# Optimization experiments

Measured on AMD Instinct MI355X. Metric: run time of the kernel, lower is better.

Reference implementation:

```python
import jax, jax.numpy as jnp
import numpy as np

N = 100000      # kg_E, number of entities
D = 256         # rel_dim
E = 1600000     # total COO edges (all batches concatenated)


def setup_inputs() -> dict:
    key = jax.random.key(0)
    ks = jax.random.split(key, 8)
    right_embed = jax.random.normal(ks[0], (N, D), dtype=jnp.float32)
    W1 = jax.random.normal(ks[1], (D, D), dtype=jnp.float32) * 0.02
    Wr = jax.random.normal(ks[2], (D, D), dtype=jnp.float32) * 0.02
    br = jax.random.normal(ks[3], (D,), dtype=jnp.float32) * 0.02
    edge_vals = jax.random.uniform(ks[4], (E,), dtype=jnp.float32)  # 1/(deg+1) weights
    edge_rows = jnp.sort(jax.random.randint(ks[5], (E,), 0, N))
    edge_cols = jax.random.randint(ks[6], (E,), 0, N)
    perm = jax.random.randint(ks[7], (N,), 0, N)  # ent_newid_tensor
    return {"right_embed": right_embed, "W1": W1, "Wr": Wr, "br": br,
            "edge_vals": edge_vals, "edge_rows": edge_rows,
            "edge_cols": edge_cols, "perm": perm}


def reference(right_embed, W1, Wr, br, edge_vals, edge_rows, edge_cols, perm):
    # add_diag_layer: dense transform then normalized-adjacency SpMM + ReLU
    h = right_embed @ W1                                   # [N, D]
    msg = edge_vals[:, None] * h[edge_cols]                # [E, D] gather
    agg = jax.ops.segment_sum(msg, edge_rows, num_segments=N)  # scatter-add
    gcn_e_1 = jax.nn.relu(agg)                             # [N, D]
    # highway gate blend with permuted input embeddings
    left = right_embed[perm]                               # [N, D]
    gate = jax.nn.sigmoid(left @ Wr + br)                  # [N, D]
    return gate * gcn_e_1 + (1.0 - gate) * left
```

## Files before the change

kernel.cpp:

```cpp
#include <hip/hip_runtime.h>
#include <hip/hip_bf16.h>
#include <math.h>

#define D 256

typedef short s16x8 __attribute__((ext_vector_type(8)));
typedef float f32x4 __attribute__((ext_vector_type(4)));

__device__ __forceinline__ unsigned short f2bf(float f) {
    unsigned int u = __builtin_bit_cast(unsigned int, f);
    unsigned int r = (u + 0x7fffu + ((u >> 16) & 1u)) >> 16;
    return (unsigned short)r;
}
__device__ __forceinline__ float bf2f(unsigned short s) {
    unsigned int u = ((unsigned int)s) << 16;
    return __builtin_bit_cast(float, u);
}

__global__ void pre_all(const float* __restrict__ X,
                        const float* __restrict__ W1, const float* __restrict__ Wr,
                        unsigned short* __restrict__ Xbf,
                        unsigned short* __restrict__ W1sw, unsigned short* __restrict__ Wrsw,
                        const int* __restrict__ rows, int* __restrict__ rp,
                        int N, int E, int rpBlocks) {
    int bid = blockIdx.x;
    if (bid < 512) {
        int idx = bid * 256 + threadIdx.x;
        int m = idx >> 16;
        int t = idx & 65535;
        const float* src = m ? Wr : W1;
        unsigned short* dst = m ? Wrsw : W1sw;
        int j = t & 7, lane = (t >> 3) & 63, nt = (t >> 9) & 15, kt = t >> 13;
        int k = kt * 32 + (lane >> 4) * 8 + j;
        int n = nt * 16 + (lane & 15);
        dst[t] = f2bf(src[k * D + n]);
    } else if (bid < 512 + rpBlocks) {
        int r = (bid - 512) * 256 + threadIdx.x;
        if (r > N) return;
        int lo = 0, hi = E;
        while (lo < hi) {
            int mid = (lo + hi) >> 1;
            if (rows[mid] < r) lo = mid + 1; else hi = mid;
        }
        rp[r] = lo;
    } else {
        long long c = (long long)(bid - 512 - rpBlocks) * 256 + threadIdx.x;
        long long i8 = c * 8;
        if (i8 >= (long long)N * D) return;
        float4 f0 = *(const float4*)(X + i8);
        float4 f1 = *(const float4*)(X + i8 + 4);
        s16x8 sf;
        sf[0] = (short)f2bf(f0.x); sf[1] = (short)f2bf(f0.y);
        sf[2] = (short)f2bf(f0.z); sf[3] = (short)f2bf(f0.w);
        sf[4] = (short)f2bf(f1.x); sf[5] = (short)f2bf(f1.y);
        sf[6] = (short)f2bf(f1.z); sf[7] = (short)f2bf(f1.w);
        *(s16x8*)(Xbf + i8) = sf;
    }
}

__device__ __forceinline__ void acc4(float4& a, uint2 u, float v) {
    float x0 = __builtin_bit_cast(float, u.x << 16);
    float x1 = __builtin_bit_cast(float, u.x & 0xffff0000u);
    float x2 = __builtin_bit_cast(float, u.y << 16);
    float x3 = __builtin_bit_cast(float, u.y & 0xffff0000u);
    a.x += v * x0; a.y += v * x1; a.z += v * x2; a.w += v * x3;
}

__global__ __launch_bounds__(256) void scatter_x(const uint2* __restrict__ xp,
                                                 const int* __restrict__ rp,
                                                 const int* __restrict__ cols,
                                                 const float* __restrict__ vals,
                                                 uint2* __restrict__ aggp,
                                                 int N, int E) {
    int lane = threadIdx.x & 63;
    int wave = threadIdx.x >> 6;
    int row = blockIdx.x * 4 + wave;
    if (row >= N) return;
    int start = rp[row], end = rp[row + 1];

    float4 a = {0.f, 0.f, 0.f, 0.f};
    for (int base = start; base < end; base += 64) {
        int ii = base + lane;
        int iic = ii < E ? ii : E - 1;
        int cl = cols[iic];
        int vbits = __builtin_bit_cast(int, vals[iic]);
        int n = end - base; if (n > 64) n = 64;
        int i = 0;
        for (; i + 8 <= n; i += 8) {
            uint2 u[8]; float vv[8];
#pragma unroll
            for (int k = 0; k < 8; k++) {
                int c = __builtin_amdgcn_readlane(cl, i + k);
                vv[k] = __builtin_bit_cast(float, __builtin_amdgcn_readlane(vbits, i + k));
                u[k] = xp[(size_t)c * 64 + lane];
            }
#pragma unroll
            for (int k = 0; k < 8; k++) acc4(a, u[k], vv[k]);
        }
        for (; i < n; i++) {
            int c = __builtin_amdgcn_readlane(cl, i);
            float v = __builtin_bit_cast(float, __builtin_amdgcn_readlane(vbits, i));
            uint2 u = xp[(size_t)c * 64 + lane];
            acc4(a, u, v);
        }
    }
    uint2 o;
    o.x = (unsigned int)f2bf(a.x) | ((unsigned int)f2bf(a.y) << 16);
    o.y = (unsigned int)f2bf(a.z) | ((unsigned int)f2bf(a.w) << 16);
    aggp[(size_t)row * 64 + lane] = o;
}

__global__ __launch_bounds__(512, 4) void gemm_ff(const unsigned short* __restrict__ aggX,
                                                  const unsigned short* __restrict__ Xbf,
                                                  const int* __restrict__ perm,
                                                  const unsigned short* __restrict__ W1sw,
                                                  const unsigned short* __restrict__ Wrsw,
                                                  const float* __restrict__ br,
                                                  float* __restrict__ out,
                                                  int N, int numTiles) {
    __shared__ unsigned short lA[8 * 64 * 16];
    int t = threadIdx.x;
    int lane = t & 63;
    int wave = t >> 6;
    int quad = lane >> 4;
    int tile = blockIdx.x;
    if (tile >= numTiles) return;

#pragma unroll
    for (int q = 0; q < 2; q++) {
        int fgi = q * 512 + t;
        int mt = fgi >> 9, kt = (fgi >> 6) & 7, ll = fgi & 63;
        int rl = ll & 15, qd = ll >> 4;
        int grow = tile * 32 + mt * 16 + rl;
        if (grow >= N) grow = N - 1;
        int pr = perm[grow];
        *(s16x8*)(lA + (size_t)fgi * 8) = *(const s16x8*)(Xbf + (size_t)pr * D + kt * 32 + qd * 8);
    }

    s16x8 bfr[2][8];
#pragma unroll
    for (int ntl = 0; ntl < 2; ntl++) {
        int nt = wave * 2 + ntl;
#pragma unroll
        for (int kt = 0; kt < 8; kt++)
            bfr[ntl][kt] = *(const s16x8*)(W1sw + ((size_t)((kt * 16 + nt) * 64 + lane)) * 8);
    }
    f32x4 acc1[2][2];
#pragma unroll
    for (int mt = 0; mt < 2; mt++)
#pragma unroll
        for (int ntl = 0; ntl < 2; ntl++) acc1[mt][ntl] = (f32x4){0.f, 0.f, 0.f, 0.f};

#pragma unroll
    for (int mt = 0; mt < 2; mt++) {
        int grow = tile * 32 + mt * 16 + (lane & 15);
        if (grow >= N) grow = N - 1;
        const unsigned short* ap = aggX + (size_t)grow * D + (lane >> 4) * 8;
#pragma unroll
        for (int kt = 0; kt < 8; kt++) {
            s16x8 a = *(const s16x8*)(ap + kt * 32);
            acc1[mt][0] = __builtin_amdgcn_mfma_f32_16x16x32_bf16(a, bfr[0][kt], acc1[mt][0], 0, 0, 0);
            acc1[mt][1] = __builtin_amdgcn_mfma_f32_16x16x32_bf16(a, bfr[1][kt], acc1[mt][1], 0, 0, 0);
        }
    }
    __syncthreads();

#pragma unroll
    for (int ntl = 0; ntl < 2; ntl++) {
        int nt = wave * 2 + ntl;
#pragma unroll
        for (int kt = 0; kt < 8; kt++)
            bfr[ntl][kt] = *(const s16x8*)(Wrsw + ((size_t)((kt * 16 + nt) * 64 + lane)) * 8);
    }
    f32x4 acc2[2][2];
#pragma unroll
    for (int mt = 0; mt < 2; mt++)
#pragma unroll
        for (int ntl = 0; ntl < 2; ntl++) acc2[mt][ntl] = (f32x4){0.f, 0.f, 0.f, 0.f};

#pragma unroll
    for (int mt = 0; mt < 2; mt++)
#pragma unroll
        for (int kt = 0; kt < 8; kt++) {
            s16x8 a = *(const s16x8*)(lA + (size_t)(((mt * 8 + kt) * 64 + lane)) * 8);
            acc2[mt][0] = __builtin_amdgcn_mfma_f32_16x16x32_bf16(a, bfr[0][kt], acc2[mt][0], 0, 0, 0);
            acc2[mt][1] = __builtin_amdgcn_mfma_f32_16x16x32_bf16(a, bfr[1][kt], acc2[mt][1], 0, 0, 0);
        }

#pragma unroll
    for (int mt = 0; mt < 2; mt++) {
#pragma unroll
        for (int ntl = 0; ntl < 2; ntl++) {
            int col = (wave * 2 + ntl) * 16 + (lane & 15);
            float b = br[col];
            int kt2 = col >> 5, qd2 = (col >> 3) & 3, j2 = col & 7;
#pragma unroll
            for (int r = 0; r < 4; r++) {
                int rt = mt * 16 + quad * 4 + r;
                int grow = tile * 32 + rt;
                if (grow < N) {
                    float pre = acc2[mt][ntl][r] + b;
                    float gate = 1.f / (1.f + __expf(-pre));
                    float gcn = fmaxf(acc1[mt][ntl][r], 0.f);
                    float left = bf2f(lA[(size_t)(((mt * 8 + kt2) * 64 + qd2 * 16 + (rt & 15))) * 8 + j2]);
                    out[(size_t)grow * D + col] = gate * gcn + (1.f - gate) * left;
                }
            }
        }
    }
}

extern "C" void kernel_launch(void* const* d_in, const int* in_sizes, int n_in,
                              void* d_out, int out_size, void* d_ws, size_t ws_size,
                              hipStream_t stream) {
    const float* right = (const float*)d_in[0];
    const float* W1    = (const float*)d_in[1];
    const float* Wr    = (const float*)d_in[2];
    const float* br    = (const float*)d_in[3];
    const float* evals = (const float*)d_in[4];
    const int*   erows = (const int*)d_in[5];
    const int*   ecols = (const int*)d_in[6];
    const int*   perm  = (const int*)d_in[7];
    int N = in_sizes[7];
    int E = in_sizes[4];
    float* out = (float*)d_out;

    char* ws = (char*)d_ws;
    unsigned short* W1sw = (unsigned short*)ws;
    unsigned short* Wrsw = W1sw + D * D;
    int* rp = (int*)(ws + (size_t)2 * D * D * 2);
    size_t off = (size_t)2 * D * D * 2 + 4 * (size_t)(N + 1);
    off = (off + 255) & ~(size_t)255;
    unsigned short* Xbf = (unsigned short*)(ws + off);
    unsigned short* aggX = Xbf + (size_t)N * D;

    int numTiles = (N + 31) / 32;
    int rpBlocks = (N + 256) / 256;
    long long cvtElems = (long long)N * D / 8;
    int cvtBlocks = (int)((cvtElems + 255) / 256);

    pre_all<<<512 + rpBlocks + cvtBlocks, 256, 0, stream>>>(right, W1, Wr, Xbf, W1sw, Wrsw,
                                                            erows, rp, N, E, rpBlocks);
    scatter_x<<<(N + 3) / 4, 256, 0, stream>>>((const uint2*)Xbf, rp, ecols, evals,
                                               (uint2*)aggX, N, E);
    gemm_ff<<<numTiles, 512, 0, stream>>>(aggX, Xbf, perm, W1sw, Wrsw, br, out, N, numTiles);
}
```

Before: 395.1 us.

## Process two row tiles per block in fused GEMM to reuse weight fragments

Each block of the final fused kernel now handles two 32-row tiles instead of one. W1 and Wr fragments are loaded into registers once and used for both tiles, halving weight-load traffic per tile. The ReLU'd first-GEMM result is packed to bf16 in registers so both tiles' outputs can be kept until the gate phase. This adds LDS use (two tiles of gathered rows), rounds the GCN term to bf16, and drops the occupancy hint, which may cut the number of resident blocks.

```diff
diff --git a/kernel.cpp b/kernel.cpp
--- a/kernel.cpp
+++ b/kernel.cpp
@@ -110,31 +110,35 @@
     aggp[(size_t)row * 64 + lane] = o;
 }
 
-__global__ __launch_bounds__(512, 4) void gemm_ff(const unsigned short* __restrict__ aggX,
-                                                  const unsigned short* __restrict__ Xbf,
-                                                  const int* __restrict__ perm,
-                                                  const unsigned short* __restrict__ W1sw,
-                                                  const unsigned short* __restrict__ Wrsw,
-                                                  const float* __restrict__ br,
-                                                  float* __restrict__ out,
-                                                  int N, int numTiles) {
-    __shared__ unsigned short lA[8 * 64 * 16];
+__global__ __launch_bounds__(512) void gemm_ff2(const unsigned short* __restrict__ aggX,
+                                                const unsigned short* __restrict__ Xbf,
+                                                const int* __restrict__ perm,
+                                                const unsigned short* __restrict__ W1sw,
+                                                const unsigned short* __restrict__ Wrsw,
+                                                const float* __restrict__ br,
+                                                float* __restrict__ out,
+                                                int N, int numTiles) {
+    __shared__ unsigned short lA[2][8192];
     int t = threadIdx.x;
     int lane = t & 63;
     int wave = t >> 6;
     int quad = lane >> 4;
-    int tile = blockIdx.x;
-    if (tile >= numTiles) return;
-
-#pragma unroll
-    for (int q = 0; q < 2; q++) {
-        int fgi = q * 512 + t;
-        int mt = fgi >> 9, kt = (fgi >> 6) & 7, ll = fgi & 63;
-        int rl = ll & 15, qd = ll >> 4;
-        int grow = tile * 32 + mt * 16 + rl;
-        if (grow >= N) grow = N - 1;
-        int pr = perm[grow];
-        *(s16x8*)(lA + (size_t)fgi * 8) = *(const s16x8*)(Xbf + (size_t)pr * D + kt * 32 + qd * 8);
+    int t0 = blockIdx.x * 2;
+    int nT = (t0 + 1 < numTiles) ? 2 : 1;
+
+    for (int tt = 0; tt < nT; tt++) {
+        int tile = t0 + tt;
+#pragma unroll
+        for (int q = 0; q < 2; q++) {
+            int fgi = q * 512 + t;
+            int mt = fgi >> 9, kt = (fgi >> 6) & 7, ll = fgi & 63;
+            int rl = ll & 15, qd = ll >> 4;
+            int grow = tile * 32 + mt * 16 + rl;
+            if (grow >= N) grow = N - 1;
+            int pr = perm[grow];
+            *(s16x8*)(&lA[tt][(size_t)fgi * 8]) =
+                *(const s16x8*)(Xbf + (size_t)pr * D + kt * 32 + qd * 8);
+        }
     }
 
     s16x8 bfr[2][8];
@@ -145,25 +149,39 @@
         for (int kt = 0; kt < 8; kt++)
             bfr[ntl][kt] = *(const s16x8*)(W1sw + ((size_t)((kt * 16 + nt) * 64 + lane)) * 8);
     }
-    f32x4 acc1[2][2];
-#pragma unroll
-    for (int mt = 0; mt < 2; mt++)
-#pragma unroll
-        for (int ntl = 0; ntl < 2; ntl++) acc1[mt][ntl] = (f32x4){0.f, 0.f, 0.f, 0.f};
-
-#pragma unroll
-    for (int mt = 0; mt < 2; mt++) {
-        int grow = tile * 32 + mt * 16 + (lane & 15);
-        if (grow >= N) grow = N - 1;
-        const unsigned short* ap = aggX + (size_t)grow * D + (lane >> 4) * 8;
-#pragma unroll
-        for (int kt = 0; kt < 8; kt++) {
-            s16x8 a = *(const s16x8*)(ap + kt * 32);
-            acc1[mt][0] = __builtin_amdgcn_mfma_f32_16x16x32_bf16(a, bfr[0][kt], acc1[mt][0], 0, 0, 0);
-            acc1[mt][1] = __builtin_amdgcn_mfma_f32_16x16x32_bf16(a, bfr[1][kt], acc1[mt][1], 0, 0, 0);
-        }
-    }
-    __syncthreads();
+
+    unsigned int g1[2][8];
+    for (int tt = 0; tt < nT; tt++) {
+        int tile = t0 + tt;
+        f32x4 acc[2][2];
+#pragma unroll
+        for (int mt = 0; mt < 2; mt++)
+#pragma unroll
+            for (int ntl = 0; ntl < 2; ntl++) acc[mt][ntl] = (f32x4){0.f, 0.f, 0.f, 0.f};
+#pragma unroll
+        for (int mt = 0; mt < 2; mt++) {
+            int grow = tile * 32 + mt * 16 + (lane & 15);
+            if (grow >= N) grow = N - 1;
+            const unsigned short* ap = aggX + (size_t)grow * D + (lane >> 4) * 8;
+#pragma unroll
+            for (int kt = 0; kt < 8; kt++) {
+                s16x8 a = *(const s16x8*)(ap + kt * 32);
+                acc[mt][0] = __builtin_amdgcn_mfma_f32_16x16x32_bf16(a, bfr[0][kt], acc[mt][0], 0, 0, 0);
+                acc[mt][1] = __builtin_amdgcn_mfma_f32_16x16x32_bf16(a, bfr[1][kt], acc[mt][1], 0, 0, 0);
+            }
+        }
+#pragma unroll
+        for (int mt = 0; mt < 2; mt++)
+#pragma unroll
+            for (int ntl = 0; ntl < 2; ntl++)
+#pragma unroll
+                for (int rp2 = 0; rp2 < 2; rp2++) {
+                    float e0 = fmaxf(acc[mt][ntl][2 * rp2], 0.f);
+                    float e1 = fmaxf(acc[mt][ntl][2 * rp2 + 1], 0.f);
+                    g1[tt][(mt * 2 + ntl) * 2 + rp2] =
+                        (unsigned int)f2bf(e0) | ((unsigned int)f2bf(e1) << 16);
+                }
+    }
 
 #pragma unroll
     for (int ntl = 0; ntl < 2; ntl++) {
@@ -172,38 +190,42 @@
         for (int kt = 0; kt < 8; kt++)
             bfr[ntl][kt] = *(const s16x8*)(Wrsw + ((size_t)((kt * 16 + nt) * 64 + lane)) * 8);
     }
-    f32x4 acc2[2][2];
-#pragma unroll
-    for (int mt = 0; mt < 2; mt++)
-#pragma unroll
-        for (int ntl = 0; ntl < 2; ntl++) acc2[mt][ntl] = (f32x4){0.f, 0.f, 0.f, 0.f};
-
-#pragma unroll
-    for (int mt = 0; mt < 2; mt++)
-#pragma unroll
-        for (int kt = 0; kt < 8; kt++) {
-            s16x8 a = *(const s16x8*)(lA + (size_t)(((mt * 8 + kt) * 64 + lane)) * 8);
-            acc2[mt][0] = __builtin_amdgcn_mfma_f32_16x16x32_bf16(a, bfr[0][kt], acc2[mt][0], 0, 0, 0);
-            acc2[mt][1] = __builtin_amdgcn_mfma_f32_16x16x32_bf16(a, bfr[1][kt], acc2[mt][1], 0, 0, 0);
-        }
-
-#pragma unroll
-    for (int mt = 0; mt < 2; mt++) {
-#pragma unroll
-        for (int ntl = 0; ntl < 2; ntl++) {
-            int col = (wave * 2 + ntl) * 16 + (lane & 15);
-            float b = br[col];
-            int kt2 = col >> 5, qd2 = (col >> 3) & 3, j2 = col & 7;
-#pragma unroll
-            for (int r = 0; r < 4; r++) {
-                int rt = mt * 16 + quad * 4 + r;
-                int grow = tile * 32 + rt;
-                if (grow < N) {
-                    float pre = acc2[mt][ntl][r] + b;
-                    float gate = 1.f / (1.f + __expf(-pre));
-                    float gcn = fmaxf(acc1[mt][ntl][r], 0.f);
-                    float left = bf2f(lA[(size_t)(((mt * 8 + kt2) * 64 + qd2 * 16 + (rt & 15))) * 8 + j2]);
-                    out[(size_t)grow * D + col] = gate * gcn + (1.f - gate) * left;
+    __syncthreads();
+
+    for (int tt = 0; tt < nT; tt++) {
+        int tile = t0 + tt;
+        f32x4 acc[2][2];
+#pragma unroll
+        for (int mt = 0; mt < 2; mt++)
+#pragma unroll
+            for (int ntl = 0; ntl < 2; ntl++) acc[mt][ntl] = (f32x4){0.f, 0.f, 0.f, 0.f};
+#pragma unroll
+        for (int mt = 0; mt < 2; mt++)
+#pragma unroll
+            for (int kt = 0; kt < 8; kt++) {
+                s16x8 a = *(const s16x8*)(&lA[tt][(size_t)(((mt * 8 + kt) * 64 + lane)) * 8]);
+                acc[mt][0] = __builtin_amdgcn_mfma_f32_16x16x32_bf16(a, bfr[0][kt], acc[mt][0], 0, 0, 0);
+                acc[mt][1] = __builtin_amdgcn_mfma_f32_16x16x32_bf16(a, bfr[1][kt], acc[mt][1], 0, 0, 0);
+            }
+#pragma unroll
+        for (int mt = 0; mt < 2; mt++) {
+#pragma unroll
+            for (int ntl = 0; ntl < 2; ntl++) {
+                int col = (wave * 2 + ntl) * 16 + (lane & 15);
+                float b = br[col];
+                int kt2 = col >> 5, qd2 = (col >> 3) & 3, j2 = col & 7;
+#pragma unroll
+                for (int r = 0; r < 4; r++) {
+                    int rt = mt * 16 + quad * 4 + r;
+                    int grow = tile * 32 + rt;
+                    if (grow < N) {
+                        float pre = acc[mt][ntl][r] + b;
+                        float gate = 1.f / (1.f + __expf(-pre));
+                        unsigned int gp = g1[tt][(mt * 2 + ntl) * 2 + (r >> 1)];
+                        float gcn = bf2f((unsigned short)((r & 1) ? (gp >> 16) : (gp & 0xffffu)));
+                        float left = bf2f(lA[tt][(size_t)(((mt * 8 + kt2) * 64 + qd2 * 16 + (rt & 15))) * 8 + j2]);
+                        out[(size_t)grow * D + col] = gate * gcn + (1.f - gate) * left;
+                    }
                 }
             }
         }
@@ -238,10 +260,11 @@
     int rpBlocks = (N + 256) / 256;
     long long cvtElems = (long long)N * D / 8;
     int cvtBlocks = (int)((cvtElems + 255) / 256);
+    int ffBlocks = (numTiles + 1) / 2;
 
     pre_all<<<512 + rpBlocks + cvtBlocks, 256, 0, stream>>>(right, W1, Wr, Xbf, W1sw, Wrsw,
                                                             erows, rp, N, E, rpBlocks);
     scatter_x<<<(N + 3) / 4, 256, 0, stream>>>((const uint2*)Xbf, rp, ecols, evals,
                                                (uint2*)aggX, N, E);
-    gemm_ff<<<numTiles, 512, 0, stream>>>(aggX, Xbf, perm, W1sw, Wrsw, br, out, N, numTiles);
-}
+    gemm_ff2<<<ffBlocks, 512, 0, stream>>>(aggX, Xbf, perm, W1sw, Wrsw, br, out, N, numTiles);
+}
```

Result: no change. 400.1 us (+1.3%).
